# Performance work log

Measured on AMD Instinct MI355X. Metric: run time of the kernel, lower is better.

## Reference

```python
import jax, jax.numpy as jnp
import numpy as np

N_NODES = 4096
IN_F = 128
HEADS = 8
HIDDEN = 8  # out_features // n_heads = 64 // 8
SLOPE = 0.2


def setup_inputs() -> dict:
    key = jax.random.key(0)
    k1, k2, k3, k4, k5 = jax.random.split(key, 5)
    h = jax.random.normal(k1, (N_NODES, IN_F), dtype=jnp.float32)
    # sparse-ish dense adjacency mask with guaranteed self-loops (avoids empty softmax rows)
    adj = jax.random.bernoulli(k2, 0.02, (N_NODES, N_NODES))
    adj = adj | jnp.eye(N_NODES, dtype=bool)
    adj = adj[:, :, None]  # [n, n, 1] as in the torch module
    W = jax.random.normal(k3, (IN_F, HEADS * HIDDEN), dtype=jnp.float32) * 0.1
    a_l = jax.random.normal(k4, (HIDDEN,), dtype=jnp.float32) * 0.1
    a_r = jax.random.normal(k5, (HIDDEN,), dtype=jnp.float32) * 0.1
    return {"h": h, "adj": adj, "W": W, "a_l": a_l, "a_r": a_r}


def reference(h, adj, W, a_l, a_r):
    n = h.shape[0]
    g = (h @ W).reshape(n, HEADS, HIDDEN)            # [n, h, d]
    # attn([g_i || g_j]) = g_i . a_l + g_j . a_r (shared across heads)
    sl = jnp.einsum('nhd,d->nh', g, a_l)             # [n, h]
    sr = jnp.einsum('nhd,d->nh', g, a_r)             # [n, h]
    e = sl[:, None, :] + sr[None, :, :]              # [n, n, h] (i = dst, j = src)
    e = jnp.where(e >= 0, e, SLOPE * e)              # leaky relu
    mask = adj[:, :, 0]                              # [n, n] bool
    e = jnp.where(mask[:, :, None], e, -jnp.inf)
    a = jax.nn.softmax(e, axis=1)                    # softmax over source nodes j
    out = jnp.einsum('ijh,jhf->ihf', a, g)           # [n, h, d]
    return out.reshape(n, HEADS * HIDDEN)            # is_concat=True
```

## Files before the change

kernel.cpp:

```cpp
#include <hip/hip_runtime.h>
#include <hip/hip_bf16.h>
#include <math.h>

#define N_NODES 4096
#define IN_F    128
#define HEADS   8
#define HIDDEN  8
#define OUTD    64
#define SLOPE   0.2f
#define WCAP    64

__global__ __launch_bounds__(256) void k1_kernel(
    const void* __restrict__ hraw, const void* __restrict__ Wraw,
    const void* __restrict__ alraw, const void* __restrict__ arraw,
    const void* __restrict__ adjraw,
    int* __restrict__ flags,
    float* __restrict__ g, float* __restrict__ slArr, float* __restrict__ srArr,
    int* __restrict__ cnt_g, int* __restrict__ edges_g) {

    __shared__ float lh[4][IN_F];
    __shared__ float lg[4][OUTD];

    const int b    = blockIdx.x;
    const int tid  = threadIdx.x;
    const int wave = tid >> 6;
    const int lane = tid & 63;

    if (b % 5 == 0) {
        const int n0 = (b / 5) * 4;

        const __hip_bfloat16* hb = (const __hip_bfloat16*)hraw;
        float p0 = __bfloat162float(hb[tid]);
        float p1 = __bfloat162float(hb[tid + 256]);
        int bad = (!(fabsf(p0) < 1e4f)) | (!(fabsf(p1) < 1e4f));
        unsigned long long bm = __ballot(bad);
        const int isF32 = (bm != 0ULL) ? 1 : 0;
        if (b == 0 && tid == 0) flags[0] = isF32;

        if (isF32) {
            const float2* hf = (const float2*)((const float*)hraw + (size_t)n0 * IN_F);
            ((float2*)&lh[0][0])[tid] = hf[tid];
        } else {
            const ushort2* h2 = (const ushort2*)((const __hip_bfloat16*)hraw + (size_t)n0 * IN_F);
            ushort2 v = h2[tid];
            float2 f;
            f.x = __bfloat162float(*(__hip_bfloat16*)&v.x);
            f.y = __bfloat162float(*(__hip_bfloat16*)&v.y);
            ((float2*)&lh[0][0])[tid] = f;
        }
        __syncthreads();

        const int nn = tid >> 6;
        const int c  = tid & 63;
        float acc = 0.f;
        if (isF32) {
            const float* Wf = (const float*)Wraw;
            #pragma unroll 8
            for (int k = 0; k < IN_F; ++k) acc += lh[nn][k] * Wf[k * OUTD + c];
        } else {
            const __hip_bfloat16* Wb = (const __hip_bfloat16*)Wraw;
            #pragma unroll 8
            for (int k = 0; k < IN_F; ++k) acc += lh[nn][k] * __bfloat162float(Wb[k * OUTD + c]);
        }
        g[(size_t)(n0 + nn) * OUTD + c] = acc;
        lg[nn][c] = acc;
        __syncthreads();

        if (tid < 32) {
            const int m  = tid >> 3;
            const int hh = tid & 7;
            float sl = 0.f, sr = 0.f;
            if (isF32) {
                const float* al = (const float*)alraw;
                const float* ar = (const float*)arraw;
                #pragma unroll
                for (int d = 0; d < HIDDEN; ++d) {
                    float gv = lg[m][hh * HIDDEN + d];
                    sl += gv * al[d]; sr += gv * ar[d];
                }
            } else {
                const __hip_bfloat16* al = (const __hip_bfloat16*)alraw;
                const __hip_bfloat16* ar = (const __hip_bfloat16*)arraw;
                #pragma unroll
                for (int d = 0; d < HIDDEN; ++d) {
                    float gv = lg[m][hh * HIDDEN + d];
                    sl += gv * __bfloat162float(al[d]); sr += gv * __bfloat162float(ar[d]);
                }
            }
            slArr[(size_t)(n0 + m) * HEADS + hh] = sl;
            srArr[(size_t)(n0 + m) * HEADS + hh] = sr;
        }
    } else {
        const int row = b - (b / 5) - 1;

        const uint4* a4 = (const uint4*)adjraw;
        uint4 det = a4[lane];
        int big = ((det.x | det.y | det.z | det.w) > 1u);
        unsigned long long dm = __ballot(big);
        const int byteadj = (dm != 0ULL) ? 1 : 0;

        unsigned int fl[16];
        if (byteadj) {
            const uint4* arow = (const uint4*)((const unsigned char*)adjraw + (size_t)row * N_NODES);
            uint4 w = arow[wave * 64 + lane];
            unsigned int wc[4] = {w.x, w.y, w.z, w.w};
            #pragma unroll
            for (int r = 0; r < 16; ++r) fl[r] = (wc[r >> 2] >> (8 * (r & 3))) & 0xFFu;
        } else {
            const uint4* arow = (const uint4*)((const int*)adjraw + (size_t)row * N_NODES);
            uint4 w0 = arow[wave * 256 + lane];
            uint4 w1 = arow[wave * 256 + 64 + lane];
            uint4 w2 = arow[wave * 256 + 128 + lane];
            uint4 w3 = arow[wave * 256 + 192 + lane];
            fl[0]=w0.x;  fl[1]=w0.y;  fl[2]=w0.z;  fl[3]=w0.w;
            fl[4]=w1.x;  fl[5]=w1.y;  fl[6]=w1.z;  fl[7]=w1.w;
            fl[8]=w2.x;  fl[9]=w2.y;  fl[10]=w2.z; fl[11]=w2.w;
            fl[12]=w3.x; fl[13]=w3.y; fl[14]=w3.z; fl[15]=w3.w;
        }

        const unsigned long long lmask = (1ULL << lane) - 1ULL;
        int* seg = edges_g + (size_t)row * (4 * WCAP) + wave * WCAP;
        int wcnt = 0;
        #pragma unroll
        for (int r = 0; r < 16; ++r) {
            unsigned long long m = __ballot(fl[r] != 0u);
            if (fl[r]) {
                int node = byteadj ? (wave * 1024 + lane * 16 + r)
                                   : (wave * 1024 + (r >> 2) * 256 + lane * 4 + (r & 3));
                int p = wcnt + (int)__popcll(m & lmask);
                if (p < WCAP) seg[p] = node;
            }
            wcnt += (int)__popcll(m);
        }
        if (lane == 0) cnt_g[row * 4 + wave] = min(wcnt, WCAP);
    }
}

__global__ __launch_bounds__(256) void k2_kernel(
    const int* __restrict__ flags,
    const float* __restrict__ g,
    const float* __restrict__ slArr, const float* __restrict__ srArr,
    const int* __restrict__ cnt_g, const int* __restrict__ edges_g,
    void* __restrict__ outraw) {

    const int i    = blockIdx.x;
    const int tid  = threadIdx.x;
    const int wave = tid >> 6;
    const int lane = tid & 63;

    __shared__ float red[4][HEADS * 9];

    const int myE = __builtin_amdgcn_readfirstlane(cnt_g[i * 4 + wave]);
    const int* seg = edges_g + (size_t)i * (4 * WCAP) + wave * WCAP;

    const int hh = lane & 7;
    const int s  = lane >> 3;
    const float sl_h = slArr[(size_t)i * HEADS + hh];

    float l = 0.f;
    float o[HIDDEN] = {0.f, 0.f, 0.f, 0.f, 0.f, 0.f, 0.f, 0.f};

    for (int e = s; e < myE; e += 8) {
        int j = seg[e];
        float x = sl_h + srArr[(size_t)j * HEADS + hh];
        x = (x >= 0.f) ? x : SLOPE * x;
        float wgt = __expf(x);
        l += wgt;
        const float4* gp = (const float4*)(g + (size_t)j * OUTD + hh * HIDDEN);
        float4 g0 = gp[0], g1 = gp[1];
        o[0] += wgt * g0.x; o[1] += wgt * g0.y; o[2] += wgt * g0.z; o[3] += wgt * g0.w;
        o[4] += wgt * g1.x; o[5] += wgt * g1.y; o[6] += wgt * g1.z; o[7] += wgt * g1.w;
    }

    #pragma unroll
    for (int m = 8; m < 64; m <<= 1) {
        l += __shfl_xor(l, m, 64);
        #pragma unroll
        for (int d = 0; d < HIDDEN; ++d) o[d] += __shfl_xor(o[d], m, 64);
    }
    if (s == 0) {
        red[wave][hh * 9 + 8] = l;
        #pragma unroll
        for (int d = 0; d < HIDDEN; ++d) red[wave][hh * 9 + d] = o[d];
    }
    __syncthreads();

    if (tid < OUTD) {
        const int h2 = tid >> 3, d2 = tid & 7;
        float os = 0.f, ls = 0.f;
        #pragma unroll
        for (int w = 0; w < 4; ++w) {
            os += red[w][h2 * 9 + d2];
            ls += red[w][h2 * 9 + 8];
        }
        float val = os / ls;
        if (flags[0]) {
            ((float*)outraw)[(size_t)i * OUTD + tid] = val;
        } else {
            ((__hip_bfloat16*)outraw)[(size_t)i * OUTD + tid] = __float2bfloat16(val);
        }
    }
}

extern "C" void kernel_launch(void* const* d_in, const int* in_sizes, int n_in,
                              void* d_out, int out_size, void* d_ws, size_t ws_size,
                              hipStream_t stream) {
    const void* h   = d_in[0];
    const void* adj = d_in[1];
    const void* W   = d_in[2];
    const void* al  = d_in[3];
    const void* ar  = d_in[4];

    char* ws = (char*)d_ws;
    size_t off = 0;
    int*   flags = (int*)(ws + off);  off += 256;
    float* g     = (float*)(ws + off); off += (size_t)N_NODES * OUTD * 4;
    float* slA   = (float*)(ws + off); off += (size_t)N_NODES * HEADS * 4;
    float* srA   = (float*)(ws + off); off += (size_t)N_NODES * HEADS * 4;
    int*   cntg  = (int*)(ws + off);   off += (size_t)N_NODES * 4 * 4;
    int*   edg   = (int*)(ws + off);   off += (size_t)N_NODES * 4 * WCAP * 4;

    k1_kernel<<<5120, 256, 0, stream>>>(h, W, al, ar, adj, flags, g, slA, srA, cntg, edg);
    k2_kernel<<<N_NODES, 256, 0, stream>>>(flags, g, slA, srA, cntg, edg, d_out);
}
```

Before: 117.1 us.

## Fuse projection and attention into one cooperative kernel with grid sync

Merges the two kernels into a single cooperative launch of 1024 blocks. Each block computes g, sl and sr for four nodes, waits on a grid-wide barrier, then has each wave handle one destination row. The edge list is built in shared memory from a per-lane bitmask with a shuffle prefix scan, and the output is written straight from the wave reduction. This removes the global edge and count buffers, the second launch and the cross-wave reduction, at the cost of a grid sync and fewer concurrent waves per row.

Measured after the change: 232.0 us. 98.2% more time.

```diff
diff --git a/kernel.cpp b/kernel.cpp
--- a/kernel.cpp
+++ b/kernel.cpp
@@ -1,6 +1,9 @@
 #include <hip/hip_runtime.h>
 #include <hip/hip_bf16.h>
+#include <hip/hip_cooperative_groups.h>
 #include <math.h>
+
+namespace cg = cooperative_groups;
 
 #define N_NODES 4096
 #define IN_F    128
@@ -8,160 +11,154 @@
 #define HIDDEN  8
 #define OUTD    64
 #define SLOPE   0.2f
-#define WCAP    64
-
-__global__ __launch_bounds__(256) void k1_kernel(
+#define ECAP    256
+
+__global__ __launch_bounds__(256, 4) void gat_fused_kernel(
     const void* __restrict__ hraw, const void* __restrict__ Wraw,
     const void* __restrict__ alraw, const void* __restrict__ arraw,
     const void* __restrict__ adjraw,
-    int* __restrict__ flags,
     float* __restrict__ g, float* __restrict__ slArr, float* __restrict__ srArr,
-    int* __restrict__ cnt_g, int* __restrict__ edges_g) {
-
-    __shared__ float lh[4][IN_F];
-    __shared__ float lg[4][OUTD];
-
-    const int b    = blockIdx.x;
+    void* __restrict__ outraw) {
+
+    __shared__ union SM {
+        struct { float lh[4][IN_F]; float lg[4][OUTD]; } a;
+        int edges[4][ECAP];
+    } sm;
+
     const int tid  = threadIdx.x;
     const int wave = tid >> 6;
     const int lane = tid & 63;
-
-    if (b % 5 == 0) {
-        const int n0 = (b / 5) * 4;
-
-        const __hip_bfloat16* hb = (const __hip_bfloat16*)hraw;
-        float p0 = __bfloat162float(hb[tid]);
-        float p1 = __bfloat162float(hb[tid + 256]);
-        int bad = (!(fabsf(p0) < 1e4f)) | (!(fabsf(p1) < 1e4f));
-        unsigned long long bm = __ballot(bad);
-        const int isF32 = (bm != 0ULL) ? 1 : 0;
-        if (b == 0 && tid == 0) flags[0] = isF32;
-
-        if (isF32) {
-            const float2* hf = (const float2*)((const float*)hraw + (size_t)n0 * IN_F);
-            ((float2*)&lh[0][0])[tid] = hf[tid];
-        } else {
-            const ushort2* h2 = (const ushort2*)((const __hip_bfloat16*)hraw + (size_t)n0 * IN_F);
-            ushort2 v = h2[tid];
-            float2 f;
-            f.x = __bfloat162float(*(__hip_bfloat16*)&v.x);
-            f.y = __bfloat162float(*(__hip_bfloat16*)&v.y);
-            ((float2*)&lh[0][0])[tid] = f;
-        }
-        __syncthreads();
-
+    const int n0   = blockIdx.x * 4;
+
+    const __hip_bfloat16* hb = (const __hip_bfloat16*)hraw;
+    float p0 = __bfloat162float(hb[tid]);
+    float p1 = __bfloat162float(hb[tid + 256]);
+    int bad = (!(fabsf(p0) < 1e4f)) | (!(fabsf(p1) < 1e4f));
+    const int isF32 = (__ballot(bad) != 0ULL) ? 1 : 0;
+
+    if (isF32) {
+        const float2* hf = (const float2*)((const float*)hraw + (size_t)n0 * IN_F);
+        ((float2*)&sm.a.lh[0][0])[tid] = hf[tid];
+    } else {
+        const ushort2* h2 = (const ushort2*)((const __hip_bfloat16*)hraw + (size_t)n0 * IN_F);
+        ushort2 v = h2[tid];
+        float2 f;
+        f.x = __bfloat162float(*(__hip_bfloat16*)&v.x);
+        f.y = __bfloat162float(*(__hip_bfloat16*)&v.y);
+        ((float2*)&sm.a.lh[0][0])[tid] = f;
+    }
+    __syncthreads();
+
+    {
         const int nn = tid >> 6;
         const int c  = tid & 63;
         float acc = 0.f;
         if (isF32) {
             const float* Wf = (const float*)Wraw;
             #pragma unroll 8
-            for (int k = 0; k < IN_F; ++k) acc += lh[nn][k] * Wf[k * OUTD + c];
+            for (int k = 0; k < IN_F; ++k) acc += sm.a.lh[nn][k] * Wf[k * OUTD + c];
         } else {
             const __hip_bfloat16* Wb = (const __hip_bfloat16*)Wraw;
             #pragma unroll 8
-            for (int k = 0; k < IN_F; ++k) acc += lh[nn][k] * __bfloat162float(Wb[k * OUTD + c]);
+            for (int k = 0; k < IN_F; ++k) acc += sm.a.lh[nn][k] * __bfloat162float(Wb[k * OUTD + c]);
         }
         g[(size_t)(n0 + nn) * OUTD + c] = acc;
-        lg[nn][c] = acc;
-        __syncthreads();
-
-        if (tid < 32) {
-            const int m  = tid >> 3;
-            const int hh = tid & 7;
-            float sl = 0.f, sr = 0.f;
-            if (isF32) {
-                const float* al = (const float*)alraw;
-                const float* ar = (const float*)arraw;
+        sm.a.lg[nn][c] = acc;
+    }
+    __syncthreads();
+
+    if (tid < 32) {
+        const int m  = tid >> 3;
+        const int hh = tid & 7;
+        float sl = 0.f, sr = 0.f;
+        if (isF32) {
+            const float* al = (const float*)alraw;
+            const float* ar = (const float*)arraw;
+            #pragma unroll
+            for (int d = 0; d < HIDDEN; ++d) {
+                float gv = sm.a.lg[m][hh * HIDDEN + d];
+                sl += gv * al[d]; sr += gv * ar[d];
+            }
+        } else {
+            const __hip_bfloat16* al = (const __hip_bfloat16*)alraw;
+            const __hip_bfloat16* ar = (const __hip_bfloat16*)arraw;
+            #pragma unroll
+            for (int d = 0; d < HIDDEN; ++d) {
+                float gv = sm.a.lg[m][hh * HIDDEN + d];
+                sl += gv * __bfloat162float(al[d]); sr += gv * __bfloat162float(ar[d]);
+            }
+        }
+        slArr[(size_t)(n0 + m) * HEADS + hh] = sl;
+        srArr[(size_t)(n0 + m) * HEADS + hh] = sr;
+    }
+
+    __threadfence();
+    cg::this_grid().sync();
+
+    const int row = n0 + wave;
+
+    const uint4* a4 = (const uint4*)adjraw;
+    uint4 det = a4[lane];
+    int big = ((det.x | det.y | det.z | det.w) > 1u);
+    const int byteadj = (__ballot(big) != 0ULL) ? 1 : 0;
+
+    unsigned long long mask = 0ULL;
+    if (byteadj) {
+        const uint4* arow = (const uint4*)((const unsigned char*)adjraw + (size_t)row * N_NODES);
+        #pragma unroll
+        for (int c = 0; c < 4; ++c) {
+            uint4 w = arow[c * 64 + lane];
+            unsigned int wc[4] = {w.x, w.y, w.z, w.w};
+            unsigned long long bits = 0ULL;
+            #pragma unroll
+            for (int k = 0; k < 4; ++k)
                 #pragma unroll
-                for (int d = 0; d < HIDDEN; ++d) {
-                    float gv = lg[m][hh * HIDDEN + d];
-                    sl += gv * al[d]; sr += gv * ar[d];
-                }
-            } else {
-                const __hip_bfloat16* al = (const __hip_bfloat16*)alraw;
-                const __hip_bfloat16* ar = (const __hip_bfloat16*)arraw;
-                #pragma unroll
-                for (int d = 0; d < HIDDEN; ++d) {
-                    float gv = lg[m][hh * HIDDEN + d];
-                    sl += gv * __bfloat162float(al[d]); sr += gv * __bfloat162float(ar[d]);
-                }
-            }
-            slArr[(size_t)(n0 + m) * HEADS + hh] = sl;
-            srArr[(size_t)(n0 + m) * HEADS + hh] = sr;
+                for (int b = 0; b < 4; ++b)
+                    if ((wc[k] >> (8 * b)) & 0xFFu) bits |= 1ULL << (k * 4 + b);
+            mask |= bits << (c * 16);
         }
     } else {
-        const int row = b - (b / 5) - 1;
-
-        const uint4* a4 = (const uint4*)adjraw;
-        uint4 det = a4[lane];
-        int big = ((det.x | det.y | det.z | det.w) > 1u);
-        unsigned long long dm = __ballot(big);
-        const int byteadj = (dm != 0ULL) ? 1 : 0;
-
-        unsigned int fl[16];
-        if (byteadj) {
-            const uint4* arow = (const uint4*)((const unsigned char*)adjraw + (size_t)row * N_NODES);
-            uint4 w = arow[wave * 64 + lane];
-            unsigned int wc[4] = {w.x, w.y, w.z, w.w};
-            #pragma unroll
-            for (int r = 0; r < 16; ++r) fl[r] = (wc[r >> 2] >> (8 * (r & 3))) & 0xFFu;
-        } else {
-            const uint4* arow = (const uint4*)((const int*)adjraw + (size_t)row * N_NODES);
-            uint4 w0 = arow[wave * 256 + lane];
-            uint4 w1 = arow[wave * 256 + 64 + lane];
-            uint4 w2 = arow[wave * 256 + 128 + lane];
-            uint4 w3 = arow[wave * 256 + 192 + lane];
-            fl[0]=w0.x;  fl[1]=w0.y;  fl[2]=w0.z;  fl[3]=w0.w;
-            fl[4]=w1.x;  fl[5]=w1.y;  fl[6]=w1.z;  fl[7]=w1.w;
-            fl[8]=w2.x;  fl[9]=w2.y;  fl[10]=w2.z; fl[11]=w2.w;
-            fl[12]=w3.x; fl[13]=w3.y; fl[14]=w3.z; fl[15]=w3.w;
-        }
-
-        const unsigned long long lmask = (1ULL << lane) - 1ULL;
-        int* seg = edges_g + (size_t)row * (4 * WCAP) + wave * WCAP;
-        int wcnt = 0;
+        const uint4* arow = (const uint4*)((const int*)adjraw + (size_t)row * N_NODES);
         #pragma unroll
-        for (int r = 0; r < 16; ++r) {
-            unsigned long long m = __ballot(fl[r] != 0u);
-            if (fl[r]) {
-                int node = byteadj ? (wave * 1024 + lane * 16 + r)
-                                   : (wave * 1024 + (r >> 2) * 256 + lane * 4 + (r & 3));
-                int p = wcnt + (int)__popcll(m & lmask);
-                if (p < WCAP) seg[p] = node;
-            }
-            wcnt += (int)__popcll(m);
-        }
-        if (lane == 0) cnt_g[row * 4 + wave] = min(wcnt, WCAP);
-    }
-}
-
-__global__ __launch_bounds__(256) void k2_kernel(
-    const int* __restrict__ flags,
-    const float* __restrict__ g,
-    const float* __restrict__ slArr, const float* __restrict__ srArr,
-    const int* __restrict__ cnt_g, const int* __restrict__ edges_g,
-    void* __restrict__ outraw) {
-
-    const int i    = blockIdx.x;
-    const int tid  = threadIdx.x;
-    const int wave = tid >> 6;
-    const int lane = tid & 63;
-
-    __shared__ float red[4][HEADS * 9];
-
-    const int myE = __builtin_amdgcn_readfirstlane(cnt_g[i * 4 + wave]);
-    const int* seg = edges_g + (size_t)i * (4 * WCAP) + wave * WCAP;
+        for (int c = 0; c < 16; ++c) {
+            uint4 w = arow[c * 64 + lane];
+            unsigned long long bits = (w.x ? 1ULL : 0ULL) | (w.y ? 2ULL : 0ULL)
+                                    | (w.z ? 4ULL : 0ULL) | (w.w ? 8ULL : 0ULL);
+            mask |= bits << (c * 4);
+        }
+    }
+
+    const int cnt = (int)__popcll(mask);
+    int pre = cnt;
+    #pragma unroll
+    for (int m2 = 1; m2 < 64; m2 <<= 1) {
+        int t = __shfl_up(pre, m2, 64);
+        if (lane >= m2) pre += t;
+    }
+    const int excl  = pre - cnt;
+    const int total = min(__builtin_amdgcn_readlane(pre, 63), ECAP);
+
+    unsigned long long mm = mask;
+    int p = excl;
+    while (mm) {
+        int k = (int)__builtin_ctzll(mm);
+        mm &= mm - 1ULL;
+        int node;
+        if (byteadj) node = ((k >> 4) * 64 + lane) * 16 + (k & 15);
+        else         node = (k >> 2) * 256 + lane * 4 + (k & 3);
+        if (p < ECAP) sm.edges[wave][p] = node;
+        ++p;
+    }
 
     const int hh = lane & 7;
     const int s  = lane >> 3;
-    const float sl_h = slArr[(size_t)i * HEADS + hh];
+    const float sl_h = slArr[(size_t)row * HEADS + hh];
 
     float l = 0.f;
     float o[HIDDEN] = {0.f, 0.f, 0.f, 0.f, 0.f, 0.f, 0.f, 0.f};
 
-    for (int e = s; e < myE; e += 8) {
-        int j = seg[e];
+    for (int e = s; e < total; e += 8) {
+        int j = sm.edges[wave][e];
         float x = sl_h + srArr[(size_t)j * HEADS + hh];
         x = (x >= 0.f) ? x : SLOPE * x;
         float wgt = __expf(x);
@@ -173,31 +170,25 @@
     }
 
     #pragma unroll
-    for (int m = 8; m < 64; m <<= 1) {
-        l += __shfl_xor(l, m, 64);
+    for (int m2 = 8; m2 < 64; m2 <<= 1) {
+        l += __shfl_xor(l, m2, 64);
         #pragma unroll
-        for (int d = 0; d < HIDDEN; ++d) o[d] += __shfl_xor(o[d], m, 64);
-    }
+        for (int d = 0; d < HIDDEN; ++d) o[d] += __shfl_xor(o[d], m2, 64);
+    }
+
     if (s == 0) {
-        red[wave][hh * 9 + 8] = l;
-        #pragma unroll
-        for (int d = 0; d < HIDDEN; ++d) red[wave][hh * 9 + d] = o[d];
-    }
-    __syncthreads();
-
-    if (tid < OUTD) {
-        const int h2 = tid >> 3, d2 = tid & 7;
-        float os = 0.f, ls = 0.f;
-        #pragma unroll
-        for (int w = 0; w < 4; ++w) {
-            os += red[w][h2 * 9 + d2];
-            ls += red[w][h2 * 9 + 8];
-        }
-        float val = os / ls;
-        if (flags[0]) {
-            ((float*)outraw)[(size_t)i * OUTD + tid] = val;
+        const float inv = 1.0f / l;
+        if (isF32) {
+            float* op = (float*)outraw + (size_t)row * OUTD + hh * HIDDEN;
+            float4 v0 = {o[0] * inv, o[1] * inv, o[2] * inv, o[3] * inv};
+            float4 v1 = {o[4] * inv, o[5] * inv, o[6] * inv, o[7] * inv};
+            ((float4*)op)[0] = v0;
+            ((float4*)op)[1] = v1;
         } else {
-            ((__hip_bfloat16*)outraw)[(size_t)i * OUTD + tid] = __float2bfloat16(val);
+            union { __hip_bfloat16 b[8]; uint4 v; } pk;
+            #pragma unroll
+            for (int d = 0; d < HIDDEN; ++d) pk.b[d] = __float2bfloat16(o[d] * inv);
+            *(uint4*)((__hip_bfloat16*)outraw + (size_t)row * OUTD + hh * HIDDEN) = pk.v;
         }
     }
 }
@@ -212,14 +203,13 @@
     const void* ar  = d_in[4];
 
     char* ws = (char*)d_ws;
-    size_t off = 0;
-    int*   flags = (int*)(ws + off);  off += 256;
-    float* g     = (float*)(ws + off); off += (size_t)N_NODES * OUTD * 4;
-    float* slA   = (float*)(ws + off); off += (size_t)N_NODES * HEADS * 4;
-    float* srA   = (float*)(ws + off); off += (size_t)N_NODES * HEADS * 4;
-    int*   cntg  = (int*)(ws + off);   off += (size_t)N_NODES * 4 * 4;
-    int*   edg   = (int*)(ws + off);   off += (size_t)N_NODES * 4 * WCAP * 4;
-
-    k1_kernel<<<5120, 256, 0, stream>>>(h, W, al, ar, adj, flags, g, slA, srA, cntg, edg);
-    k2_kernel<<<N_NODES, 256, 0, stream>>>(flags, g, slA, srA, cntg, edg, d_out);
+    size_t off = 256;
+    float* g   = (float*)(ws + off); off += (size_t)N_NODES * OUTD * 4;
+    float* slA = (float*)(ws + off); off += (size_t)N_NODES * HEADS * 4;
+    float* srA = (float*)(ws + off); off += (size_t)N_NODES * HEADS * 4;
+
+    void* args[] = {(void*)&h, (void*)&W, (void*)&al, (void*)&ar, (void*)&adj,
+                    (void*)&g, (void*)&slA, (void*)&srA, (void*)&d_out};
+    hipLaunchCooperativeKernel((const void*)gat_fused_kernel,
+                               dim3(N_NODES / 4), dim3(256), args, 0, stream);
 }
```
